# Kernel optimization log

Measured on AMD Instinct MI355X. Metric: run time of the kernel, lower is better.

The kernel has to match this reference:

```python
import jax, jax.numpy as jnp
import numpy as np

B, S, D, H = 1, 2048, 1280, 16
HD = D // H  # 80


def setup_inputs() -> dict:
    key = jax.random.key(0)
    ks = jax.random.split(key, 6)
    return {
        "hidden_states": jax.random.normal(ks[0], (B, S, D), dtype=jnp.float32),
        "rotary_pos_emb": jax.random.normal(ks[1], (S, HD // 2), dtype=jnp.float32),
        "qkv_w": jax.random.normal(ks[2], (3 * D, D), dtype=jnp.float32) * 0.02,
        "qkv_b": jax.random.normal(ks[3], (3 * D,), dtype=jnp.float32) * 0.02,
        "proj_w": jax.random.normal(ks[4], (D, D), dtype=jnp.float32) * 0.02,
        "proj_b": jax.random.normal(ks[5], (D,), dtype=jnp.float32) * 0.02,
    }


def reference(hidden_states, rotary_pos_emb, qkv_w, qkv_b, proj_w, proj_b):
    b, s, d = hidden_states.shape
    h = H
    hd = d // h
    scaling = hd ** -0.5

    # fused QKV projection: [b, s, 3*d]
    qkv = hidden_states @ qkv_w.T + qkv_b
    qkv = qkv.reshape(b, s, 3, h, hd)
    q, k, v = qkv[:, :, 0], qkv[:, :, 1], qkv[:, :, 2]  # each [b, s, h, hd]

    # rotary embedding: cos/sin [s, hd//2] -> [1, s, 1, hd]
    cos = jnp.cos(rotary_pos_emb)
    sin = jnp.sin(rotary_pos_emb)
    cos = jnp.concatenate([cos, cos], axis=-1)[None, :, None, :]
    sin = jnp.concatenate([sin, sin], axis=-1)[None, :, None, :]

    def apply_rope(x):
        x1, x2 = x[..., : hd // 2], x[..., hd // 2:]
        return x * cos + jnp.concatenate([-x2, x1], axis=-1) * sin

    q = apply_rope(q)
    k = apply_rope(k)

    # [b, h, s, hd]
    q = q.transpose(0, 2, 1, 3)
    k = k.transpose(0, 2, 1, 3)
    v = v.transpose(0, 2, 1, 3)

    # naive full attention matrix [b, h, s, s]
    attn = jnp.einsum("bhqd,bhkd->bhqk", q, k) * scaling
    attn = jax.nn.softmax(attn, axis=-1)
    out = jnp.einsum("bhqk,bhkd->bhqd", attn, v)
    out = out.transpose(0, 2, 1, 3).reshape(b, s, d)
    return out @ proj_w.T + proj_b
```

## Files before the change

### kernel.cpp

```cpp
#include <hip/hip_runtime.h>
#include <math.h>

#define SS 2048
#define DD 1280
#define HH 16
#define HDD 80
#define ND3 3840

typedef __attribute__((ext_vector_type(8))) short short8;
typedef __attribute__((ext_vector_type(4))) short s16x4;
typedef __attribute__((ext_vector_type(4))) float f32x4;
typedef __attribute__((ext_vector_type(8))) _Float16 h16x8;
typedef __attribute__((ext_vector_type(4))) _Float16 h16x4;

__device__ inline short f2bf(float f) {
    union { float f; unsigned u; } x; x.f = f;
    unsigned r = x.u + 0x7FFF + ((x.u >> 16) & 1);
    return (short)(r >> 16);
}

__global__ __launch_bounds__(256) void split_f16(
    const float* __restrict__ a, _Float16* __restrict__ ah, int nbA,
    const float* __restrict__ b, _Float16* __restrict__ bh, int nbB,
    const float* __restrict__ c, _Float16* __restrict__ ch)
{
    const float* x; _Float16* h;
    int blk = blockIdx.x;
    if (blk < nbA)            { x = a; h = ah; }
    else if (blk < nbA + nbB) { blk -= nbA; x = b; h = bh; }
    else                      { blk -= nbA + nbB; x = c; h = ch; }
    int i = (blk * 256 + threadIdx.x) * 4;
    float4 v = *(const float4*)(x + i);
    h16x4 hv;
    hv[0] = (_Float16)v.x; hv[1] = (_Float16)v.y;
    hv[2] = (_Float16)v.z; hv[3] = (_Float16)v.w;
    *(h16x4*)(h + i) = hv;
}

#define LDSA(m, kg) ((m) * 32 + (((kg) ^ (((m) >> 1) & 3)) << 3))

template <int BMT, int BNT>
__global__ __launch_bounds__(256) void gemm_f16(
    const _Float16* __restrict__ Ah, const _Float16* __restrict__ Bh,
    const float* __restrict__ bias, float* __restrict__ C,
    int M, int N, int K)
{
    constexpr int IT = BMT / 32;
    constexpr int JT = BNT / 32;
    constexpr int AU = BMT / 64;
    constexpr int BU = BNT / 64;
    __shared__ _Float16 AhS[BMT * 32];
    __shared__ _Float16 BhS[BNT * 32];

    const int tid = threadIdx.x;
    const int w = tid >> 6;
    const int lane = tid & 63;
    const int l15 = lane & 15;
    const int quad = lane >> 4;
    const int wm = w >> 1, wn = w & 1;
    const int bm = blockIdx.y * BMT;
    const int bn = blockIdx.x * BNT;

    f32x4 acc[IT][JT];
    #pragma unroll
    for (int i = 0; i < IT; ++i)
        #pragma unroll
        for (int j = 0; j < JT; ++j)
            acc[i][j] = (f32x4){0.f, 0.f, 0.f, 0.f};

    h16x8 rah[AU], rbh[BU];
    auto loadg = [&](int k0) {
        #pragma unroll
        for (int u = 0; u < AU; ++u) {
            int c = tid + u * 256, m = c >> 2, kg = c & 3;
            rah[u] = *(const h16x8*)(Ah + (size_t)(bm + m) * K + k0 + kg * 8);
        }
        #pragma unroll
        for (int u = 0; u < BU; ++u) {
            int c = tid + u * 256, m = c >> 2, kg = c & 3;
            rbh[u] = *(const h16x8*)(Bh + (size_t)(bn + m) * K + k0 + kg * 8);
        }
    };

    loadg(0);
    for (int k0 = 0; k0 < K; k0 += 32) {
        __syncthreads();
        #pragma unroll
        for (int u = 0; u < AU; ++u) {
            int c = tid + u * 256, m = c >> 2, kg = c & 3;
            *(h16x8*)&AhS[LDSA(m, kg)] = rah[u];
        }
        #pragma unroll
        for (int u = 0; u < BU; ++u) {
            int c = tid + u * 256, m = c >> 2, kg = c & 3;
            *(h16x8*)&BhS[LDSA(m, kg)] = rbh[u];
        }
        __syncthreads();
        if (k0 + 32 < K) loadg(k0 + 32);

        h16x8 af[IT], bf[JT];
        #pragma unroll
        for (int i = 0; i < IT; ++i) {
            int m = wm * (BMT / 2) + i * 16 + l15;
            af[i] = *(h16x8*)&AhS[LDSA(m, quad)];
        }
        #pragma unroll
        for (int j = 0; j < JT; ++j) {
            int n = wn * (BNT / 2) + j * 16 + l15;
            bf[j] = *(h16x8*)&BhS[LDSA(n, quad)];
        }
        #pragma unroll
        for (int i = 0; i < IT; ++i)
            #pragma unroll
            for (int j = 0; j < JT; ++j)
                acc[i][j] = __builtin_amdgcn_mfma_f32_16x16x32_f16(af[i], bf[j], acc[i][j], 0, 0, 0);
    }

    #pragma unroll
    for (int j = 0; j < JT; ++j) {
        int col = bn + wn * (BNT / 2) + j * 16 + l15;
        float bb = bias[col];
        #pragma unroll
        for (int i = 0; i < IT; ++i)
            #pragma unroll
            for (int r = 0; r < 4; ++r) {
                int row = bm + wm * (BMT / 2) + i * 16 + quad * 4 + r;
                C[(size_t)row * N + col] = acc[i][j][r] + bb;
            }
    }
}

__global__ __launch_bounds__(256) void rope_scatter_bf16(
    const float* __restrict__ qkv, const float* __restrict__ rpe,
    short* __restrict__ q, short* __restrict__ k, short* __restrict__ v)
{
    __shared__ float cs[40], sn[40];
    const int s = blockIdx.x;
    if (threadIdx.x < 40)
        __sincosf(rpe[s * 40 + threadIdx.x], &sn[threadIdx.x], &cs[threadIdx.x]);
    __syncthreads();
    const float scale = 0.11180339887498949f;
    for (int j = threadIdx.x; j < ND3; j += 256) {
        int p = j / DD;
        int rem = j - p * DD;
        int hh = rem / HDD;
        int d = rem - hh * HDD;
        float x = qkv[(size_t)s * ND3 + j];
        float val;
        if (p == 2) {
            val = x;
        } else {
            int dm = (d < 40) ? d : d - 40;
            float other = (d < 40)
                ? -qkv[(size_t)s * ND3 + p * DD + hh * HDD + d + 40]
                :  qkv[(size_t)s * ND3 + p * DD + hh * HDD + d - 40];
            val = x * cs[dm] + other * sn[dm];
            if (p == 0) val *= scale;
        }
        short* dst = (p == 0) ? q : (p == 1) ? k : v;
        dst[((size_t)hh * SS + s) * HDD + d] = f2bf(val);
    }
}

__global__ __launch_bounds__(256) void attn_mfma(
    const short* __restrict__ q, const short* __restrict__ k,
    const short* __restrict__ v, float* __restrict__ o_part,
    float* __restrict__ l_part)
{
    __shared__ short Ks[64][104];
    __shared__ short Vts[80 * 64];
    __shared__ short Ps[4][32][72];

    const int h = blockIdx.y;
    const int q0 = blockIdx.x << 7;
    const int z = blockIdx.z;
    const int tid = threadIdx.x;
    const int w = tid >> 6;
    const int lane = tid & 63;
    const int l15 = lane & 15;
    const int quad = lane >> 4;

    const short* qbase = q + (size_t)h * SS * HDD;
    const short* kbase = k + (size_t)h * SS * HDD;
    const short* vbase = v + (size_t)h * SS * HDD;

    short8 qf[2][3];
    #pragma unroll
    for (int i = 0; i < 2; ++i) {
        const int row = q0 + w * 32 + i * 16 + l15;
        #pragma unroll
        for (int kk = 0; kk < 3; ++kk) {
            int c0 = kk * 32 + quad * 8;
            qf[i][kk] = (c0 < HDD) ? *(const short8*)(qbase + (size_t)row * HDD + c0)
                                   : (short8)0;
        }
    }

    if (tid < 128) {
        int r = tid >> 1, c = 80 + (tid & 1) * 8;
        *(short8*)&Ks[r][c] = (short8)0;
    }

    float lsum[2][4] = {{0.f}};
    f32x4 o[2][5];
    #pragma unroll
    for (int i = 0; i < 2; ++i)
        #pragma unroll
        for (int n = 0; n < 5; ++n) o[i][n] = (f32x4){0.f, 0.f, 0.f, 0.f};

    const int kt0 = z << 10;
    for (int kt = kt0; kt < kt0 + 1024; kt += 64) {
        __syncthreads();
        #pragma unroll
        for (int u = 0; u < 3; ++u) {
            int i = tid + u * 256;
            if (i < 640) {
                int r = i / 10, c = (i - r * 10) * 8;
                *(short8*)&Ks[r][c] = *(const short8*)(kbase + (size_t)(kt + r) * HDD + c);
            }
        }
        #pragma unroll
        for (int u = 0; u < 2; ++u) {
            int task = tid + u * 256;
            if (task < 320) {
                int r4 = (task & 15) << 2;
                int d4 = (task >> 4) << 2;
                s16x4 a0 = *(const s16x4*)(vbase + (size_t)(kt + r4 + 0) * HDD + d4);
                s16x4 a1 = *(const s16x4*)(vbase + (size_t)(kt + r4 + 1) * HDD + d4);
                s16x4 a2 = *(const s16x4*)(vbase + (size_t)(kt + r4 + 2) * HDD + d4);
                s16x4 a3 = *(const s16x4*)(vbase + (size_t)(kt + r4 + 3) * HDD + d4);
                #pragma unroll
                for (int j = 0; j < 4; ++j) {
                    s16x4 w4 = {a0[j], a1[j], a2[j], a3[j]};
                    int d = d4 + j;
                    int sw = (r4 >> 3) ^ (d & 7);
                    *(s16x4*)&Vts[d * 64 + sw * 8 + (r4 & 7)] = w4;
                }
            }
        }
        __syncthreads();

        f32x4 s_[2][4];
        #pragma unroll
        for (int nt = 0; nt < 4; ++nt) {
            short8 bf0 = *(short8*)&Ks[nt * 16 + l15][0 * 32 + quad * 8];
            short8 bf1 = *(short8*)&Ks[nt * 16 + l15][1 * 32 + quad * 8];
            short8 bf2 = *(short8*)&Ks[nt * 16 + l15][2 * 32 + quad * 8];
            #pragma unroll
            for (int i = 0; i < 2; ++i) {
                f32x4 acc = (f32x4){0.f, 0.f, 0.f, 0.f};
                acc = __builtin_amdgcn_mfma_f32_16x16x32_bf16(qf[i][0], bf0, acc, 0, 0, 0);
                acc = __builtin_amdgcn_mfma_f32_16x16x32_bf16(qf[i][1], bf1, acc, 0, 0, 0);
                acc = __builtin_amdgcn_mfma_f32_16x16x32_bf16(qf[i][2], bf2, acc, 0, 0, 0);
                s_[i][nt] = acc;
            }
        }

        #pragma unroll
        for (int i = 0; i < 2; ++i)
            #pragma unroll
            for (int nt = 0; nt < 4; ++nt)
                #pragma unroll
                for (int r = 0; r < 4; ++r) {
                    float p = __expf(s_[i][nt][r] - 16.f);
                    lsum[i][r] += p;
                    Ps[w][i * 16 + quad * 4 + r][nt * 16 + l15] = f2bf(p);
                }

        short8 pf[2][2];
        #pragma unroll
        for (int i = 0; i < 2; ++i)
            #pragma unroll
            for (int kk = 0; kk < 2; ++kk)
                pf[i][kk] = *(short8*)&Ps[w][i * 16 + l15][kk * 32 + quad * 8];
        #pragma unroll
        for (int n = 0; n < 5; ++n) {
            #pragma unroll
            for (int kk = 0; kk < 2; ++kk) {
                int d = n * 16 + l15;
                int sw = (kk * 4 + quad) ^ (l15 & 7);
                short8 vf = *(short8*)&Vts[d * 64 + sw * 8];
                #pragma unroll
                for (int i = 0; i < 2; ++i)
                    o[i][n] = __builtin_amdgcn_mfma_f32_16x16x32_bf16(pf[i][kk], vf, o[i][n], 0, 0, 0);
            }
        }
    }

    float* ob = o_part + (size_t)z * SS * DD;
    #pragma unroll
    for (int i = 0; i < 2; ++i) {
        #pragma unroll
        for (int r = 0; r < 4; ++r) {
            float rs = lsum[i][r];
            #pragma unroll
            for (int off = 1; off < 16; off <<= 1)
                rs += __shfl_xor(rs, off, 64);
            lsum[i][r] = rs;
        }
        #pragma unroll
        for (int n = 0; n < 5; ++n)
            #pragma unroll
            for (int r = 0; r < 4; ++r) {
                int row = q0 + w * 32 + i * 16 + quad * 4 + r;
                ob[(size_t)row * DD + h * HDD + n * 16 + l15] = o[i][n][r];
            }
        if (l15 == 0)
            #pragma unroll
            for (int r = 0; r < 4; ++r)
                l_part[((size_t)z * HH + h) * SS + q0 + w * 32 + i * 16 + quad * 4 + r] = lsum[i][r];
    }
}

__global__ __launch_bounds__(256) void attn_merge(
    const float* __restrict__ o_part, const float* __restrict__ l_part,
    _Float16* __restrict__ oh)
{
    int i = (blockIdx.x * 256 + threadIdx.x) * 4;
    int row = i / DD;
    int col = i - row * DD;
    int h = col / HDD;
    float4 a = *(const float4*)(o_part + i);
    float4 b = *(const float4*)(o_part + (size_t)SS * DD + i);
    float l = l_part[h * SS + row] + l_part[(HH + h) * SS + row];
    float inv = 1.f / l;
    h16x4 hv;
    hv[0] = (_Float16)((a.x + b.x) * inv);
    hv[1] = (_Float16)((a.y + b.y) * inv);
    hv[2] = (_Float16)((a.z + b.z) * inv);
    hv[3] = (_Float16)((a.w + b.w) * inv);
    *(h16x4*)(oh + i) = hv;
}

extern "C" void kernel_launch(void* const* d_in, const int* in_sizes, int n_in,
                              void* d_out, int out_size, void* d_ws, size_t ws_size,
                              hipStream_t stream)
{
    const float* hs     = (const float*)d_in[0];
    const float* rpe    = (const float*)d_in[1];
    const float* qkv_w  = (const float*)d_in[2];
    const float* qkv_b  = (const float*)d_in[3];
    const float* proj_w = (const float*)d_in[4];
    const float* proj_b = (const float*)d_in[5];
    float* out = (float*)d_out;

    short* s0 = (short*)d_ws;
    float* qkv_f  = (float*)d_ws;
    float* o_part = (float*)d_ws;
    float* l_part = (float*)d_ws + 5242880;
    short* s1 = s0 + 15728640;
    _Float16* qkvw_h = (_Float16*)s1;
    short* qb = s1;
    short* kb = s1 + 2621440;
    short* vb = s1 + 5242880;
    _Float16* attn_h = (_Float16*)s1;
    short* s2 = s1 + 7864320;
    _Float16* hs_h = (_Float16*)s2;
    _Float16* projw_h = (_Float16*)s2;

    const int n_hs = SS * DD;
    const int n_qw = ND3 * DD;
    const int n_pw = DD * DD;

    split_f16<<<n_hs / 1024 + n_qw / 1024, 256, 0, stream>>>(
        hs, hs_h, n_hs / 1024,
        qkv_w, qkvw_h, n_qw / 1024,
        qkv_w, qkvw_h);
    gemm_f16<128, 128><<<dim3(ND3 / 128, SS / 128), 256, 0, stream>>>(
        hs_h, qkvw_h, qkv_b, qkv_f, SS, ND3, DD);
    split_f16<<<n_pw / 1024, 256, 0, stream>>>(
        proj_w, projw_h, n_pw / 1024,
        proj_w, projw_h, 0,
        proj_w, projw_h);
    rope_scatter_bf16<<<SS, 256, 0, stream>>>(qkv_f, rpe, qb, kb, vb);
    attn_mfma<<<dim3(SS / 128, HH, 2), 256, 0, stream>>>(qb, kb, vb, o_part, l_part);
    attn_merge<<<(SS * DD) / 1024, 256, 0, stream>>>(o_part, l_part, attn_h);
    gemm_f16<64, 128><<<dim3(DD / 128, SS / 64), 256, 0, stream>>>(
        attn_h, projw_h, proj_b, out, SS, DD, DD);
}
```

Baseline: 217.3 us.

## Split-K QKV GEMM and four-way KV split in attention with fp16 partials

The QKV GEMM gets a split-K variant with two K halves. It writes fp16 partial outputs that the rope kernel sums, which doubles the block count and halves the intermediate bytes. Attention now splits the key range four ways instead of two for more parallelism, and stores partial outputs in fp16. The merge kernel combines the four partials. The K tile LDS padding shrinks, the Q fragment loads skip the out-of-range chunk, and the fixed softmax offset changes from 16 to 8. The fp16 partials and the fixed max offset carry overflow and precision risk.

```diff
diff --git a/kernel.cpp b/kernel.cpp
--- a/kernel.cpp
+++ b/kernel.cpp
@@ -40,10 +40,10 @@
 #define LDSA(m, kg) ((m) * 32 + (((kg) ^ (((m) >> 1) & 3)) << 3))
 
 template <int BMT, int BNT>
-__global__ __launch_bounds__(256) void gemm_f16(
+__global__ __launch_bounds__(256) void gemm_f16_sk(
     const _Float16* __restrict__ Ah, const _Float16* __restrict__ Bh,
-    const float* __restrict__ bias, float* __restrict__ C,
-    int M, int N, int K)
+    const float* __restrict__ bias, _Float16* __restrict__ Cp,
+    int M, int N, int K, int Kh)
 {
     constexpr int IT = BMT / 32;
     constexpr int JT = BNT / 32;
@@ -60,6 +60,8 @@
     const int wm = w >> 1, wn = w & 1;
     const int bm = blockIdx.y * BMT;
     const int bn = blockIdx.x * BNT;
+    const int z = blockIdx.z;
+    const int kbeg = z * Kh, kend = kbeg + Kh;
 
     f32x4 acc[IT][JT];
     #pragma unroll
@@ -82,8 +84,8 @@
         }
     };
 
-    loadg(0);
-    for (int k0 = 0; k0 < K; k0 += 32) {
+    loadg(kbeg);
+    for (int k0 = kbeg; k0 < kend; k0 += 32) {
         __syncthreads();
         #pragma unroll
         for (int u = 0; u < AU; ++u) {
@@ -96,7 +98,7 @@
             *(h16x8*)&BhS[LDSA(m, kg)] = rbh[u];
         }
         __syncthreads();
-        if (k0 + 32 < K) loadg(k0 + 32);
+        if (k0 + 32 < kend) loadg(k0 + 32);
 
         h16x8 af[IT], bf[JT];
         #pragma unroll
@@ -116,6 +118,98 @@
                 acc[i][j] = __builtin_amdgcn_mfma_f32_16x16x32_f16(af[i], bf[j], acc[i][j], 0, 0, 0);
     }
 
+    _Float16* C = Cp + (size_t)z * M * N;
+    #pragma unroll
+    for (int j = 0; j < JT; ++j) {
+        int col = bn + wn * (BNT / 2) + j * 16 + l15;
+        float bb = (z == 0) ? bias[col] : 0.f;
+        #pragma unroll
+        for (int i = 0; i < IT; ++i)
+            #pragma unroll
+            for (int r = 0; r < 4; ++r) {
+                int row = bm + wm * (BMT / 2) + i * 16 + quad * 4 + r;
+                C[(size_t)row * N + col] = (_Float16)(acc[i][j][r] + bb);
+            }
+    }
+}
+
+template <int BMT, int BNT>
+__global__ __launch_bounds__(256) void gemm_f16(
+    const _Float16* __restrict__ Ah, const _Float16* __restrict__ Bh,
+    const float* __restrict__ bias, float* __restrict__ C,
+    int M, int N, int K)
+{
+    constexpr int IT = BMT / 32;
+    constexpr int JT = BNT / 32;
+    constexpr int AU = BMT / 64;
+    constexpr int BU = BNT / 64;
+    __shared__ _Float16 AhS[BMT * 32];
+    __shared__ _Float16 BhS[BNT * 32];
+
+    const int tid = threadIdx.x;
+    const int w = tid >> 6;
+    const int lane = tid & 63;
+    const int l15 = lane & 15;
+    const int quad = lane >> 4;
+    const int wm = w >> 1, wn = w & 1;
+    const int bm = blockIdx.y * BMT;
+    const int bn = blockIdx.x * BNT;
+
+    f32x4 acc[IT][JT];
+    #pragma unroll
+    for (int i = 0; i < IT; ++i)
+        #pragma unroll
+        for (int j = 0; j < JT; ++j)
+            acc[i][j] = (f32x4){0.f, 0.f, 0.f, 0.f};
+
+    h16x8 rah[AU], rbh[BU];
+    auto loadg = [&](int k0) {
+        #pragma unroll
+        for (int u = 0; u < AU; ++u) {
+            int c = tid + u * 256, m = c >> 2, kg = c & 3;
+            rah[u] = *(const h16x8*)(Ah + (size_t)(bm + m) * K + k0 + kg * 8);
+        }
+        #pragma unroll
+        for (int u = 0; u < BU; ++u) {
+            int c = tid + u * 256, m = c >> 2, kg = c & 3;
+            rbh[u] = *(const h16x8*)(Bh + (size_t)(bn + m) * K + k0 + kg * 8);
+        }
+    };
+
+    loadg(0);
+    for (int k0 = 0; k0 < K; k0 += 32) {
+        __syncthreads();
+        #pragma unroll
+        for (int u = 0; u < AU; ++u) {
+            int c = tid + u * 256, m = c >> 2, kg = c & 3;
+            *(h16x8*)&AhS[LDSA(m, kg)] = rah[u];
+        }
+        #pragma unroll
+        for (int u = 0; u < BU; ++u) {
+            int c = tid + u * 256, m = c >> 2, kg = c & 3;
+            *(h16x8*)&BhS[LDSA(m, kg)] = rbh[u];
+        }
+        __syncthreads();
+        if (k0 + 32 < K) loadg(k0 + 32);
+
+        h16x8 af[IT], bf[JT];
+        #pragma unroll
+        for (int i = 0; i < IT; ++i) {
+            int m = wm * (BMT / 2) + i * 16 + l15;
+            af[i] = *(h16x8*)&AhS[LDSA(m, quad)];
+        }
+        #pragma unroll
+        for (int j = 0; j < JT; ++j) {
+            int n = wn * (BNT / 2) + j * 16 + l15;
+            bf[j] = *(h16x8*)&BhS[LDSA(n, quad)];
+        }
+        #pragma unroll
+        for (int i = 0; i < IT; ++i)
+            #pragma unroll
+            for (int j = 0; j < JT; ++j)
+                acc[i][j] = __builtin_amdgcn_mfma_f32_16x16x32_f16(af[i], bf[j], acc[i][j], 0, 0, 0);
+    }
+
     #pragma unroll
     for (int j = 0; j < JT; ++j) {
         int col = bn + wn * (BNT / 2) + j * 16 + l15;
@@ -131,7 +225,8 @@
 }
 
 __global__ __launch_bounds__(256) void rope_scatter_bf16(
-    const float* __restrict__ qkv, const float* __restrict__ rpe,
+    const _Float16* __restrict__ p0, const _Float16* __restrict__ p1,
+    const float* __restrict__ rpe,
     short* __restrict__ q, short* __restrict__ k, short* __restrict__ v)
 {
     __shared__ float cs[40], sn[40];
@@ -145,16 +240,17 @@
         int rem = j - p * DD;
         int hh = rem / HDD;
         int d = rem - hh * HDD;
-        float x = qkv[(size_t)s * ND3 + j];
+        size_t base = (size_t)s * ND3;
+        float x = (float)p0[base + j] + (float)p1[base + j];
         float val;
         if (p == 2) {
             val = x;
         } else {
             int dm = (d < 40) ? d : d - 40;
-            float other = (d < 40)
-                ? -qkv[(size_t)s * ND3 + p * DD + hh * HDD + d + 40]
-                :  qkv[(size_t)s * ND3 + p * DD + hh * HDD + d - 40];
-            val = x * cs[dm] + other * sn[dm];
+            size_t oi = base + p * DD + hh * HDD + ((d < 40) ? d + 40 : d - 40);
+            float oth = (float)p0[oi] + (float)p1[oi];
+            if (d < 40) oth = -oth;
+            val = x * cs[dm] + oth * sn[dm];
             if (p == 0) val *= scale;
         }
         short* dst = (p == 0) ? q : (p == 1) ? k : v;
@@ -164,10 +260,10 @@
 
 __global__ __launch_bounds__(256) void attn_mfma(
     const short* __restrict__ q, const short* __restrict__ k,
-    const short* __restrict__ v, float* __restrict__ o_part,
+    const short* __restrict__ v, _Float16* __restrict__ o_part,
     float* __restrict__ l_part)
 {
-    __shared__ short Ks[64][104];
+    __shared__ short Ks[64][88];
     __shared__ short Vts[80 * 64];
     __shared__ short Ps[4][32][72];
 
@@ -188,18 +284,14 @@
     #pragma unroll
     for (int i = 0; i < 2; ++i) {
         const int row = q0 + w * 32 + i * 16 + l15;
-        #pragma unroll
-        for (int kk = 0; kk < 3; ++kk) {
-            int c0 = kk * 32 + quad * 8;
-            qf[i][kk] = (c0 < HDD) ? *(const short8*)(qbase + (size_t)row * HDD + c0)
-                                   : (short8)0;
-        }
-    }
-
-    if (tid < 128) {
-        int r = tid >> 1, c = 80 + (tid & 1) * 8;
-        *(short8*)&Ks[r][c] = (short8)0;
-    }
+        qf[i][0] = *(const short8*)(qbase + (size_t)row * HDD + quad * 8);
+        qf[i][1] = *(const short8*)(qbase + (size_t)row * HDD + 32 + quad * 8);
+        qf[i][2] = (quad < 2) ? *(const short8*)(qbase + (size_t)row * HDD + 64 + quad * 8)
+                              : (short8)0;
+    }
+
+    if (tid < 64)
+        *(short8*)&Ks[tid][80] = (short8)0;
 
     float lsum[2][4] = {{0.f}};
     f32x4 o[2][5];
@@ -208,8 +300,8 @@
         #pragma unroll
         for (int n = 0; n < 5; ++n) o[i][n] = (f32x4){0.f, 0.f, 0.f, 0.f};
 
-    const int kt0 = z << 10;
-    for (int kt = kt0; kt < kt0 + 1024; kt += 64) {
+    const int kt0 = z << 9;
+    for (int kt = kt0; kt < kt0 + 512; kt += 64) {
         __syncthreads();
         #pragma unroll
         for (int u = 0; u < 3; ++u) {
@@ -243,9 +335,9 @@
         f32x4 s_[2][4];
         #pragma unroll
         for (int nt = 0; nt < 4; ++nt) {
-            short8 bf0 = *(short8*)&Ks[nt * 16 + l15][0 * 32 + quad * 8];
-            short8 bf1 = *(short8*)&Ks[nt * 16 + l15][1 * 32 + quad * 8];
-            short8 bf2 = *(short8*)&Ks[nt * 16 + l15][2 * 32 + quad * 8];
+            short8 bf0 = *(short8*)&Ks[nt * 16 + l15][quad * 8];
+            short8 bf1 = *(short8*)&Ks[nt * 16 + l15][32 + quad * 8];
+            short8 bf2 = *(short8*)&Ks[nt * 16 + l15][64 + quad * 8];
             #pragma unroll
             for (int i = 0; i < 2; ++i) {
                 f32x4 acc = (f32x4){0.f, 0.f, 0.f, 0.f};
@@ -262,7 +354,7 @@
             for (int nt = 0; nt < 4; ++nt)
                 #pragma unroll
                 for (int r = 0; r < 4; ++r) {
-                    float p = __expf(s_[i][nt][r] - 16.f);
+                    float p = __expf(s_[i][nt][r] - 8.f);
                     lsum[i][r] += p;
                     Ps[w][i * 16 + quad * 4 + r][nt * 16 + l15] = f2bf(p);
                 }
@@ -287,7 +379,7 @@
         }
     }
 
-    float* ob = o_part + (size_t)z * SS * DD;
+    _Float16* ob = o_part + (size_t)z * SS * DD;
     #pragma unroll
     for (int i = 0; i < 2; ++i) {
         #pragma unroll
@@ -303,7 +395,7 @@
             #pragma unroll
             for (int r = 0; r < 4; ++r) {
                 int row = q0 + w * 32 + i * 16 + quad * 4 + r;
-                ob[(size_t)row * DD + h * HDD + n * 16 + l15] = o[i][n][r];
+                ob[(size_t)row * DD + h * HDD + n * 16 + l15] = (_Float16)o[i][n][r];
             }
         if (l15 == 0)
             #pragma unroll
@@ -313,22 +405,28 @@
 }
 
 __global__ __launch_bounds__(256) void attn_merge(
-    const float* __restrict__ o_part, const float* __restrict__ l_part,
+    const _Float16* __restrict__ o_part, const float* __restrict__ l_part,
     _Float16* __restrict__ oh)
 {
     int i = (blockIdx.x * 256 + threadIdx.x) * 4;
     int row = i / DD;
     int col = i - row * DD;
     int h = col / HDD;
-    float4 a = *(const float4*)(o_part + i);
-    float4 b = *(const float4*)(o_part + (size_t)SS * DD + i);
-    float l = l_part[h * SS + row] + l_part[(HH + h) * SS + row];
+    float l = 0.f;
+    float acc[4] = {0.f, 0.f, 0.f, 0.f};
+    #pragma unroll
+    for (int zz = 0; zz < 4; ++zz) {
+        l += l_part[(zz * HH + h) * SS + row];
+        h16x4 a = *(const h16x4*)(o_part + (size_t)zz * SS * DD + i);
+        acc[0] += (float)a[0]; acc[1] += (float)a[1];
+        acc[2] += (float)a[2]; acc[3] += (float)a[3];
+    }
     float inv = 1.f / l;
     h16x4 hv;
-    hv[0] = (_Float16)((a.x + b.x) * inv);
-    hv[1] = (_Float16)((a.y + b.y) * inv);
-    hv[2] = (_Float16)((a.z + b.z) * inv);
-    hv[3] = (_Float16)((a.w + b.w) * inv);
+    hv[0] = (_Float16)(acc[0] * inv);
+    hv[1] = (_Float16)(acc[1] * inv);
+    hv[2] = (_Float16)(acc[2] * inv);
+    hv[3] = (_Float16)(acc[3] * inv);
     *(h16x4*)(oh + i) = hv;
 }
 
@@ -345,9 +443,9 @@
     float* out = (float*)d_out;
 
     short* s0 = (short*)d_ws;
-    float* qkv_f  = (float*)d_ws;
-    float* o_part = (float*)d_ws;
-    float* l_part = (float*)d_ws + 5242880;
+    _Float16* qkv_p = (_Float16*)s0;
+    _Float16* o_part = (_Float16*)s0;
+    float* l_part = (float*)(s0 + 10485760);
     short* s1 = s0 + 15728640;
     _Float16* qkvw_h = (_Float16*)s1;
     short* qb = s1;
@@ -366,14 +464,15 @@
         hs, hs_h, n_hs / 1024,
         qkv_w, qkvw_h, n_qw / 1024,
         qkv_w, qkvw_h);
-    gemm_f16<128, 128><<<dim3(ND3 / 128, SS / 128), 256, 0, stream>>>(
-        hs_h, qkvw_h, qkv_b, qkv_f, SS, ND3, DD);
+    gemm_f16_sk<128, 128><<<dim3(ND3 / 128, SS / 128, 2), 256, 0, stream>>>(
+        hs_h, qkvw_h, qkv_b, qkv_p, SS, ND3, DD, DD / 2);
     split_f16<<<n_pw / 1024, 256, 0, stream>>>(
         proj_w, projw_h, n_pw / 1024,
         proj_w, projw_h, 0,
         proj_w, projw_h);
-    rope_scatter_bf16<<<SS, 256, 0, stream>>>(qkv_f, rpe, qb, kb, vb);
-    attn_mfma<<<dim3(SS / 128, HH, 2), 256, 0, stream>>>(qb, kb, vb, o_part, l_part);
+    rope_scatter_bf16<<<SS, 256, 0, stream>>>(
+        qkv_p, qkv_p + (size_t)SS * ND3, rpe, qb, kb, vb);
+    attn_mfma<<<dim3(SS / 128, HH, 4), 256, 0, stream>>>(qb, kb, vb, o_part, l_part);
     attn_merge<<<(SS * DD) / 1024, 256, 0, stream>>>(o_part, l_part, attn_h);
     gemm_f16<64, 128><<<dim3(DD / 128, SS / 64), 256, 0, stream>>>(
         attn_h, projw_h, proj_b, out, SS, DD, DD);
```

Measured after the change: 228.9 us. 1.05x slower.
